# Kernel optimization log

Hardware: AMD Instinct MI355X
Metric: run time of the kernel (lower is better)

## Reference

```python
import jax, jax.numpy as jnp
import numpy as np

WH, WW = 7, 7
N = WH * WW
DIM = 384
HEADS = 12
NW = 64          # windows per image
B_ = 2048        # batch * NW


def _relative_position_index():
    ch, cw = np.meshgrid(np.arange(WH), np.arange(WW), indexing='ij')
    coords = np.stack([ch, cw]).reshape(2, -1)                      # [2, N]
    rel = coords[:, :, None] - coords[:, None, :]                   # [2, N, N]
    rel = rel.transpose(1, 2, 0)
    rel[:, :, 0] += WH - 1
    rel[:, :, 1] += WW - 1
    rel[:, :, 0] *= 2 * WW - 1
    return jnp.asarray(rel.sum(-1), dtype=jnp.int32)                # [N, N]


def setup_inputs() -> dict:
    key = jax.random.key(0)
    ks = jax.random.split(key, 7)
    return {
        'x': jax.random.normal(ks[0], (B_, N, DIM), dtype=jnp.float32),
        'qkv_w': jax.random.normal(ks[1], (3 * DIM, DIM), dtype=jnp.float32) * 0.02,
        'qkv_b': jax.random.normal(ks[2], (3 * DIM,), dtype=jnp.float32) * 0.02,
        'proj_w': jax.random.normal(ks[3], (DIM, DIM), dtype=jnp.float32) * 0.02,
        'proj_b': jax.random.normal(ks[4], (DIM,), dtype=jnp.float32) * 0.02,
        'bias_table': jax.random.normal(ks[5], ((2 * WH - 1) * (2 * WW - 1), HEADS), dtype=jnp.float32) * 0.02,
        'mask': jax.random.normal(ks[6], (NW, N, N), dtype=jnp.float32),
        'rel_idx': _relative_position_index(),
    }


def reference(x, qkv_w, qkv_b, proj_w, proj_b, bias_table, mask, rel_idx):
    B_, n, C = x.shape
    H = HEADS
    hd = C // H
    scale = hd ** (-0.5)

    qkv = x @ qkv_w.T + qkv_b                                        # [B_, N, 3C]
    qkv = qkv.reshape(B_, n, 3, H, hd).transpose(2, 0, 3, 1, 4)      # [3, B_, H, N, hd]
    q, k, v = qkv[0], qkv[1], qkv[2]

    attn = jnp.einsum('bhqd,bhkd->bhqk', q * scale, k)               # [B_, H, N, N]

    rpb = bias_table[rel_idx.reshape(-1)].reshape(n, n, H)           # gather [N, N, H]
    attn = attn + rpb.transpose(2, 0, 1)[None]                       # [B_, H, N, N]

    nW = mask.shape[0]
    attn = attn.reshape(B_ // nW, nW, H, n, n) + mask[None, :, None]
    attn = attn.reshape(B_, H, n, n)
    attn = jax.nn.softmax(attn, axis=-1)

    out = jnp.einsum('bhqk,bhkd->bhqd', attn, v)                     # [B_, H, N, hd]
    out = out.transpose(0, 2, 1, 3).reshape(B_, n, C)
    return out @ proj_w.T + proj_b
```

## Files before the change

kernel.cpp:

```cpp
#include <hip/hip_runtime.h>
#include <hip/hip_bf16.h>
#include <cstdint>
#include <cstddef>

#define NTOK 49
#define DIM 384
#define KDIM 384
#define HEADS 12
#define HD 32
#define BATCH 2048
#define MROWS (BATCH * NTOK)

typedef unsigned short u16;
typedef __bf16 bf16x8 __attribute__((ext_vector_type(8)));
typedef unsigned short u16x8 __attribute__((ext_vector_type(8)));
typedef float f32x4 __attribute__((ext_vector_type(4)));
typedef float f32x16 __attribute__((ext_vector_type(16)));

__device__ __forceinline__ u16 f2b(float f) {
  union { float f; unsigned u; } v; v.f = f;
  unsigned r = v.u + 0x7fffu + ((v.u >> 16) & 1u);
  return (u16)(r >> 16);
}

__device__ __forceinline__ bf16x8 ld_bf8(const u16* p) {
  u16x8 u = *(const u16x8*)p;
  return __builtin_bit_cast(bf16x8, u);
}

__device__ __forceinline__ void gload_lds16(const void* g, void* l) {
  __builtin_amdgcn_global_load_lds(
      (const __attribute__((address_space(1))) unsigned*)g,
      (__attribute__((address_space(3))) unsigned*)l, 16, 0, 0);
}

__global__ __launch_bounds__(256) void k_prep(const float* __restrict__ x,
                                              u16* __restrict__ xb,
                                              const float* __restrict__ qkv_w,
                                              u16* __restrict__ wqkvb,
                                              const float* __restrict__ proj_w,
                                              u16* __restrict__ wprojb,
                                              const float* __restrict__ bias_table,
                                              const float* __restrict__ mask,
                                              const int* __restrict__ rel_idx,
                                              float* __restrict__ rpbm) {
  int blk = blockIdx.x;
  if (blk < 38208) {
    const float* in;
    u16* out;
    int i;
    if (blk < 37632) {
      in = x; out = xb; i = blk * 256 + threadIdx.x;
    } else if (blk < 38064) {
      in = qkv_w; out = wqkvb; i = (blk - 37632) * 256 + threadIdx.x;
    } else {
      in = proj_w; out = wprojb; i = (blk - 38064) * 256 + threadIdx.x;
    }
    float4 v = ((const float4*)in)[i];
    ushort4 o;
    o.x = f2b(v.x); o.y = f2b(v.y); o.z = f2b(v.z); o.w = f2b(v.w);
    ((ushort4*)out)[i] = o;
  } else {
    int gidx = (blk - 38208) * 256 + threadIdx.x;
    int l    = gidx & 63;
    int rq   = (gidx >> 6) & 3;
    int tile = (gidx >> 8) & 3;
    int w    = (gidx >> 10) & 63;
    int h    = gidx >> 16;
    int mi = tile >> 1, nj = tile & 1;
    int kk0 = mi * 32 + 8 * rq + 4 * (l >> 5);
    int qq  = nj * 32 + (l & 31);
    float4 out;
    float* op = (float*)&out;
#pragma unroll
    for (int rl = 0; rl < 4; ++rl) {
      int kk = kk0 + rl;
      float v = -1e30f;
      if (kk < NTOK && qq < NTOK)
        v = bias_table[rel_idx[qq * NTOK + kk] * HEADS + h] +
            mask[(w * NTOK + qq) * NTOK + kk];
      op[rl] = v;
    }
    ((float4*)rpbm)[gidx] = out;
  }
}

template <int OUT_BF16, int NCOLS, int NTN, int GD8>
__global__ __launch_bounds__(512, 4) void k_gemm256(const u16* __restrict__ A,
                                                    const u16* __restrict__ B,
                                                    const float* __restrict__ bias,
                                                    void* __restrict__ Cv,
                                                    long m_base) {
  __shared__ u16 sh[36864];
  int bid = blockIdx.x;
  int tile = (bid & 7) * GD8 + (bid >> 3);
  int mt = tile / NTN, nt = tile - mt * NTN;
  long m0 = m_base + (long)mt * 256;
  int n0 = nt * 128;
  int tid = threadIdx.x;
  int lane = tid & 63, wid = tid >> 6;
  int wr = (wid >> 1) * 64, wc = (wid & 1) * 64;
  int c = lane & 15, g = lane >> 4;
  int gsw = (g ^ ((c >> 1) & 3)) * 8;

  int srow = wid * 16 + (lane >> 2);
  int scol = ((lane & 3) ^ ((lane >> 3) & 3)) * 8;
  const u16* gA = A + (m0 + srow) * (long)KDIM + scol;
  const u16* gB = B + (long)(n0 + srow) * KDIM + scol;
  int lrow = srow, lseg = (lane & 3) * 8;

  f32x4 acc[4][4] = {};
  bf16x8 af[4], bfr[4];

#define STAGE256(BUF, KT)                                                      \
  {                                                                            \
    u16* As_ = sh + (BUF) * 12288;                                             \
    u16* Bs_ = As_ + 8192;                                                     \
    gload_lds16(gA + (KT), &As_[lrow * 32 + lseg]);                            \
    gload_lds16(gA + (KT) + 128L * KDIM, &As_[(lrow + 128) * 32 + lseg]);      \
    gload_lds16(gB + (KT), &Bs_[lrow * 32 + lseg]);                            \
  }

#define FRAGREAD(BUF)                                                          \
  {                                                                            \
    const u16* As = sh + (BUF) * 12288;                                        \
    const u16* Bs = As + 8192;                                                 \
    _Pragma("unroll") for (int i = 0; i < 4; ++i) {                            \
      af[i]  = ld_bf8(&As[(wr + i * 16 + c) * 32 + gsw]);                      \
      bfr[i] = ld_bf8(&Bs[(wc + i * 16 + c) * 32 + gsw]);                      \
    }                                                                          \
  }

#define MFMA_CL                                                                \
  __builtin_amdgcn_s_setprio(1);                                               \
  _Pragma("unroll") for (int mi = 0; mi < 4; ++mi)                             \
  _Pragma("unroll") for (int ni = 0; ni < 4; ++ni)                             \
      acc[mi][ni] = __builtin_amdgcn_mfma_f32_16x16x32_bf16(                   \
          af[mi], bfr[ni], acc[mi][ni], 0, 0, 0);                              \
  __builtin_amdgcn_s_setprio(0);

#define GITER(T, NV)                                                           \
  {                                                                            \
    MFMA_CL;                                                                   \
    asm volatile("s_waitcnt vmcnt(" #NV ")" ::: "memory");                     \
    __builtin_amdgcn_s_barrier();                                              \
    __builtin_amdgcn_sched_barrier(0);                                         \
    if ((T) + 3 < 12) STAGE256((T) % 3, ((T) + 3) * 32);                       \
    FRAGREAD(((T) + 1) % 3);                                                   \
  }

  STAGE256(0, 0);
  STAGE256(1, 32);
  STAGE256(2, 64);
  asm volatile("s_waitcnt vmcnt(6)" ::: "memory");
  __builtin_amdgcn_s_barrier();
  __builtin_amdgcn_sched_barrier(0);
  FRAGREAD(0);

  GITER(0, 3)  GITER(1, 3)  GITER(2, 3)  GITER(3, 3)
  GITER(4, 3)  GITER(5, 3)  GITER(6, 3)  GITER(7, 3)
  GITER(8, 3)  GITER(9, 3)  GITER(10, 0)
  { MFMA_CL; }
  __builtin_amdgcn_s_barrier();
#undef GITER
#undef MFMA_CL
#undef FRAGREAD
#undef STAGE256

  if (OUT_BF16) {
    u16* C = (u16*)Cv;
#pragma unroll
    for (int mi = 0; mi < 4; ++mi)
#pragma unroll
      for (int ni = 0; ni < 4; ++ni) {
        int col = wc + ni * 16 + c;
        float bv = bias[n0 + col];
#pragma unroll
        for (int r = 0; r < 4; ++r) {
          int row = wr + mi * 16 + g * 4 + r;
          sh[row * 128 + col] = f2b(acc[mi][ni][r] + bv);
        }
      }
    __syncthreads();
#pragma unroll
    for (int rep = 0; rep < 8; ++rep) {
      int idx = rep * 4096 + tid * 8;
      int row = idx >> 7, col = idx & 127;
      int grow = (int)m0 + row;
      int b = grow / 49, tok = grow - b * 49;
      int gcol = n0 + col;
      int t = gcol / 384;
      int hc = gcol - t * 384;
      int h = hc >> 5, d0 = hc & 31;
      size_t off = (((size_t)(t * 12 + h) * BATCH + b) * 49 + tok) * 32 + d0;
      *(u16x8*)(C + off) = *(const u16x8*)&sh[idx];
    }
  } else {
    float* C = (float*)Cv;
    float* shf = (float*)sh;
#pragma unroll
    for (int chunk = 0; chunk < 2; ++chunk) {
      __syncthreads();
      if ((wid >> 2) == chunk) {
#pragma unroll
        for (int mi = 0; mi < 4; ++mi)
#pragma unroll
          for (int ni = 0; ni < 4; ++ni) {
            int col = wc + ni * 16 + c;
            float bv = bias[n0 + col];
#pragma unroll
            for (int r = 0; r < 4; ++r) {
              int lr = ((wid >> 1) & 1) * 64 + mi * 16 + g * 4 + r;
              shf[lr * 128 + col] = acc[mi][ni][r] + bv;
            }
          }
      }
      __syncthreads();
#pragma unroll
      for (int rep = 0; rep < 8; ++rep) {
        int idx = rep * 2048 + tid * 4;
        int row = idx >> 7, col = idx & 127;
        *(float4*)(C + (m0 + chunk * 128 + row) * NCOLS + n0 + col) =
            *(const float4*)&shf[idx];
      }
    }
  }
}

__global__ __launch_bounds__(256) void k_attn(const u16* __restrict__ qkv,
                                              const float* __restrict__ rpbmT,
                                              u16* __restrict__ attnout) {
  __shared__ u16 vT_lds[4][32 * 64];
  int lane = threadIdx.x & 63, wid = threadIdx.x >> 6;
  int blk = blockIdx.x;
  int w = blk / 96;
  int rr = blk - w * 96;
  int j = rr / 3;
  int hb = rr - j * 3;
  int b = j * 64 + w;
  int h = hb * 4 + wid;
  int l31 = lane & 31, hi = lane >> 5;

  const u16* qh = qkv + ((size_t)(h)*BATCH + b) * (49 * 32);
  const u16* kh = qkv + ((size_t)(12 + h) * BATCH + b) * (49 * 32);
  const u16* vh = qkv + ((size_t)(24 + h) * BATCH + b) * (49 * 32);

  u16x8 vv[4];
#pragma unroll
  for (int t = 0; t < 4; ++t) {
    int idx = t * 64 + lane;
    int jj = idx >> 2, d0 = (idx & 3) * 8;
    int jr = jj < NTOK ? jj : NTOK - 1;
    vv[t] = *(const u16x8*)(vh + jr * 32 + d0);
  }
  bf16x8 kf[2][2], qf[2][2];
#pragma unroll
  for (int mi = 0; mi < 2; ++mi) {
    int row = mi * 32 + l31; if (row > NTOK - 1) row = NTOK - 1;
#pragma unroll
    for (int k2 = 0; k2 < 2; ++k2)
      kf[mi][k2] = ld_bf8(kh + row * 32 + k2 * 16 + hi * 8);
  }
#pragma unroll
  for (int nj = 0; nj < 2; ++nj) {
    int row = nj * 32 + l31; if (row > NTOK - 1) row = NTOK - 1;
#pragma unroll
    for (int k2 = 0; k2 < 2; ++k2)
      qf[nj][k2] = ld_bf8(qh + row * 32 + k2 * 16 + hi * 8);
  }

  u16* vt = vT_lds[wid];
#pragma unroll
  for (int t = 0; t < 4; ++t) {
    int idx = t * 64 + lane;
    int jj = idx >> 2, d0 = (idx & 3) * 8;
#pragma unroll
    for (int dd = 0; dd < 8; ++dd) {
      int d = d0 + dd;
      int byte = (d * 128 + jj * 2) ^ ((d & 7) << 4);
      *(u16*)((char*)vt + byte) = (u16)vv[t][dd];
    }
  }

  f32x16 s[2][2];
  f32x16 z16 = {};
#pragma unroll
  for (int mi = 0; mi < 2; ++mi)
#pragma unroll
    for (int nj = 0; nj < 2; ++nj) {
      s[mi][nj] = __builtin_amdgcn_mfma_f32_32x32x16_bf16(kf[mi][0], qf[nj][0],
                                                          z16, 0, 0, 0);
      s[mi][nj] = __builtin_amdgcn_mfma_f32_32x32x16_bf16(kf[mi][1], qf[nj][1],
                                                          s[mi][nj], 0, 0, 0);
    }

  const float scale = 0.17677669529663687f;
  const f32x4* rp = (const f32x4*)(rpbmT + ((size_t)(h * 64 + w)) * 4096);
#pragma unroll
  for (int mi = 0; mi < 2; ++mi)
#pragma unroll
    for (int nj = 0; nj < 2; ++nj)
#pragma unroll
      for (int rq = 0; rq < 4; ++rq) {
        f32x4 rv = rp[(mi * 2 + nj) * 256 + rq * 64 + lane];
#pragma unroll
        for (int rl = 0; rl < 4; ++rl)
          s[mi][nj][rq * 4 + rl] = s[mi][nj][rq * 4 + rl] * scale + rv[rl];
      }

  float inv_[2];
#pragma unroll
  for (int nj = 0; nj < 2; ++nj) {
    float mx = s[0][nj][0];
#pragma unroll
    for (int mi = 0; mi < 2; ++mi)
#pragma unroll
      for (int r = 0; r < 16; ++r)
        mx = fmaxf(mx, s[mi][nj][r]);
    mx = fmaxf(mx, __shfl_xor(mx, 32));
    float sum = 0.f;
#pragma unroll
    for (int mi = 0; mi < 2; ++mi)
#pragma unroll
      for (int r = 0; r < 16; ++r) {
        float p = __expf(s[mi][nj][r] - mx);
        s[mi][nj][r] = p;
        sum += p;
      }
    sum += __shfl_xor(sum, 32);
    inv_[nj] = __builtin_amdgcn_rcpf(sum);
  }

  asm volatile("s_waitcnt lgkmcnt(0)" ::: "memory");
  __builtin_amdgcn_sched_barrier(0);

  f32x16 o[2] = {};
#pragma unroll
  for (int kk = 0; kk < 4; ++kk) {
    int byte = (l31 * 128 + kk * 32 + hi * 16) ^ ((l31 & 7) << 4);
    bf16x8 va = __builtin_bit_cast(bf16x8, *(const u16x8*)((const char*)vt + byte));
#pragma unroll
    for (int nj = 0; nj < 2; ++nj) {
      const int mi = kk >> 1, br = (kk & 1) * 8;
      unsigned t0, t1, t2, t3;
      asm("v_cvt_pk_bf16_f32 %0, %1, %2"
          : "=v"(t0) : "v"(s[mi][nj][br + 0]), "v"(s[mi][nj][br + 1]));
      asm("v_cvt_pk_bf16_f32 %0, %1, %2"
          : "=v"(t1) : "v"(s[mi][nj][br + 2]), "v"(s[mi][nj][br + 3]));
      asm("v_cvt_pk_bf16_f32 %0, %1, %2"
          : "=v"(t2) : "v"(s[mi][nj][br + 4]), "v"(s[mi][nj][br + 5]));
      asm("v_cvt_pk_bf16_f32 %0, %1, %2"
          : "=v"(t3) : "v"(s[mi][nj][br + 6]), "v"(s[mi][nj][br + 7]));
      asm("v_permlane32_swap_b32 %0, %1" : "+v"(t0), "+v"(t2));
      asm("v_permlane32_swap_b32 %0, %1" : "+v"(t1), "+v"(t3));
      uint4 uu; uu.x = t0; uu.y = t1; uu.z = t2; uu.w = t3;
      bf16x8 pb = __builtin_bit_cast(bf16x8, uu);
      o[nj] = __builtin_amdgcn_mfma_f32_32x32x16_bf16(va, pb, o[nj], 0, 0, 0);
    }
  }

  u16* obase = attnout + (size_t)b * (NTOK * DIM) + h * HD;
#pragma unroll
  for (int nj = 0; nj < 2; ++nj) {
    int q = nj * 32 + l31;
    if (q < NTOK) {
#pragma unroll
      for (int r = 0; r < 16; ++r) {
        int d = (r & 3) + 8 * (r >> 2) + 4 * hi;
        obase[(size_t)q * DIM + d] = f2b(o[nj][r] * inv_[nj]);
      }
    }
  }
}

extern "C" void kernel_launch(void* const* d_in, const int* in_sizes, int n_in,
                              void* d_out, int out_size, void* d_ws, size_t ws_size,
                              hipStream_t stream) {
  const float* x       = (const float*)d_in[0];
  const float* qkv_w   = (const float*)d_in[1];
  const float* qkv_b   = (const float*)d_in[2];
  const float* proj_w  = (const float*)d_in[3];
  const float* proj_b  = (const float*)d_in[4];
  const float* bias_tb = (const float*)d_in[5];
  const float* mask    = (const float*)d_in[6];
  const int*   rel_idx = (const int*)d_in[7];
  float* out = (float*)d_out;

  char* ws = (char*)d_ws;
  u16*   xb      = (u16*)(ws + 0);
  u16*   wqkvb   = (u16*)(ws + 77070336);
  u16*   wprojb  = (u16*)(ws + 77955072);
  float* rpbm    = (float*)(ws + 78249984);
  u16*   qkv     = (u16*)(ws + 90832896);
  u16*   attnout = (u16*)(ws + 322043904);

  k_prep<<<41280, 256, 0, stream>>>(x, xb, qkv_w, wqkvb, proj_w, wprojb,
                                    bias_tb, mask, rel_idx, rpbm);

  k_gemm256<1, 1152, 9, 225><<<1800, 512, 0, stream>>>(xb, wqkvb, qkv_b,
                                                       (void*)qkv, 0L);
  k_gemm256<1, 1152, 9, 216><<<1728, 512, 0, stream>>>(xb, wqkvb, qkv_b,
                                                       (void*)qkv, 51200L);

  k_attn<<<6144, 256, 0, stream>>>(qkv, rpbm, attnout);

  k_gemm256<0, 384, 3, 147><<<1176, 512, 0, stream>>>(attnout, wprojb, proj_b,
                                                      (void*)out, 0L);

  (void)in_sizes; (void)n_in; (void)out_size; (void)ws_size;
}
```

Measured before the change: 354.1 us.

## Write V pre-transposed from QKV GEMM and drop LDS transpose in attention

The QKV GEMM epilogue now writes the V third transposed, as [head][batch][d][token padded to 56], through a swizzled LDS staging step. The attention kernel then loads V fragments straight from global memory, with no per-wave LDS transpose or waitcnt barrier. The 49th token is handled by a separate mostly-zero MFMA, and output stores become 4-wide vectors. The two QKV GEMM launches are merged into one, and attnout reuses the xb workspace region. The trade-off is scalar 2-byte global stores in the V epilogue, which may be uncoalesced and slow.

```diff
diff --git a/kernel.cpp b/kernel.cpp
--- a/kernel.cpp
+++ b/kernel.cpp
@@ -10,6 +10,7 @@
 #define HD 32
 #define BATCH 2048
 #define MROWS (BATCH * NTOK)
+#define VPAD 56
 
 typedef unsigned short u16;
 typedef __bf16 bf16x8 __attribute__((ext_vector_type(8)));
@@ -90,12 +91,12 @@
                                                     const u16* __restrict__ B,
                                                     const float* __restrict__ bias,
                                                     void* __restrict__ Cv,
-                                                    long m_base) {
+                                                    u16* __restrict__ Cv2) {
   __shared__ u16 sh[36864];
   int bid = blockIdx.x;
   int tile = (bid & 7) * GD8 + (bid >> 3);
   int mt = tile / NTN, nt = tile - mt * NTN;
-  long m0 = m_base + (long)mt * 256;
+  long m0 = (long)mt * 256;
   int n0 = nt * 128;
   int tid = threadIdx.x;
   int lane = tid & 63, wid = tid >> 6;
@@ -168,32 +169,66 @@
 #undef STAGE256
 
   if (OUT_BF16) {
-    u16* C = (u16*)Cv;
-#pragma unroll
-    for (int mi = 0; mi < 4; ++mi)
-#pragma unroll
-      for (int ni = 0; ni < 4; ++ni) {
-        int col = wc + ni * 16 + c;
-        float bv = bias[n0 + col];
-#pragma unroll
-        for (int r = 0; r < 4; ++r) {
-          int row = wr + mi * 16 + g * 4 + r;
-          sh[row * 128 + col] = f2b(acc[mi][ni][r] + bv);
+    if (n0 < 768) {
+      u16* C = (u16*)Cv;
+#pragma unroll
+      for (int mi = 0; mi < 4; ++mi)
+#pragma unroll
+        for (int ni = 0; ni < 4; ++ni) {
+          int col = wc + ni * 16 + c;
+          float bv = bias[n0 + col];
+#pragma unroll
+          for (int r = 0; r < 4; ++r) {
+            int row = wr + mi * 16 + g * 4 + r;
+            sh[row * 128 + col] = f2b(acc[mi][ni][r] + bv);
+          }
         }
-      }
-    __syncthreads();
-#pragma unroll
-    for (int rep = 0; rep < 8; ++rep) {
-      int idx = rep * 4096 + tid * 8;
-      int row = idx >> 7, col = idx & 127;
-      int grow = (int)m0 + row;
-      int b = grow / 49, tok = grow - b * 49;
-      int gcol = n0 + col;
-      int t = gcol / 384;
-      int hc = gcol - t * 384;
-      int h = hc >> 5, d0 = hc & 31;
-      size_t off = (((size_t)(t * 12 + h) * BATCH + b) * 49 + tok) * 32 + d0;
-      *(u16x8*)(C + off) = *(const u16x8*)&sh[idx];
+      __syncthreads();
+#pragma unroll
+      for (int rep = 0; rep < 8; ++rep) {
+        int idx = rep * 4096 + tid * 8;
+        int row = idx >> 7, col = idx & 127;
+        int grow = (int)m0 + row;
+        int b = grow / 49, tok = grow - b * 49;
+        int gcol = n0 + col;
+        int t = gcol / 384;
+        int hc = gcol - t * 384;
+        int h = hc >> 5, d0 = hc & 31;
+        size_t off = (((size_t)(t * 12 + h) * BATCH + b) * 49 + tok) * 32 + d0;
+        *(u16x8*)(C + off) = *(const u16x8*)&sh[idx];
+      }
+    } else {
+#pragma unroll
+      for (int mi = 0; mi < 4; ++mi)
+#pragma unroll
+        for (int ni = 0; ni < 4; ++ni) {
+          int col = wc + ni * 16 + c;
+          float bv = bias[n0 + col];
+          int sw = (col & 7) << 3;
+#pragma unroll
+          for (int r = 0; r < 4; ++r) {
+            int row = wr + mi * 16 + g * 4 + r;
+            sh[col * 256 + (row ^ sw)] = f2b(acc[mi][ni][r] + bv);
+          }
+        }
+      __syncthreads();
+#pragma unroll
+      for (int rep = 0; rep < 8; ++rep) {
+        int idx = rep * 4096 + tid * 8;
+        int dloc = idx >> 8, rowb = idx & 255;
+        u16x8 vals = *(const u16x8*)&sh[dloc * 256 + (rowb ^ ((dloc & 7) << 3))];
+        int hcol = n0 - 768 + dloc;
+        int h = hcol >> 5, d = hcol & 31;
+        int grow = (int)m0 + rowb;
+        int b = grow / 49, j = grow - b * 49;
+        size_t off = ((size_t)(h * BATCH + b) * 32 + d) * VPAD + j;
+#pragma unroll
+        for (int e = 0; e < 8; ++e) {
+          Cv2[off] = (u16)vals[e];
+          ++j; ++off;
+          if (j == 49) { j = 0; ++b; off += (size_t)32 * VPAD - 49; }
+        }
+      }
     }
   } else {
     float* C = (float*)Cv;
@@ -227,10 +262,10 @@
   }
 }
 
-__global__ __launch_bounds__(256) void k_attn(const u16* __restrict__ qkv,
+__global__ __launch_bounds__(256) void k_attn(const u16* __restrict__ qkvqk,
+                                              const u16* __restrict__ vtg,
                                               const float* __restrict__ rpbmT,
                                               u16* __restrict__ attnout) {
-  __shared__ u16 vT_lds[4][32 * 64];
   int lane = threadIdx.x & 63, wid = threadIdx.x >> 6;
   int blk = blockIdx.x;
   int w = blk / 96;
@@ -241,18 +276,16 @@
   int h = hb * 4 + wid;
   int l31 = lane & 31, hi = lane >> 5;
 
-  const u16* qh = qkv + ((size_t)(h)*BATCH + b) * (49 * 32);
-  const u16* kh = qkv + ((size_t)(12 + h) * BATCH + b) * (49 * 32);
-  const u16* vh = qkv + ((size_t)(24 + h) * BATCH + b) * (49 * 32);
-
-  u16x8 vv[4];
-#pragma unroll
-  for (int t = 0; t < 4; ++t) {
-    int idx = t * 64 + lane;
-    int jj = idx >> 2, d0 = (idx & 3) * 8;
-    int jr = jj < NTOK ? jj : NTOK - 1;
-    vv[t] = *(const u16x8*)(vh + jr * 32 + d0);
-  }
+  const u16* qh = qkvqk + ((size_t)(h)*BATCH + b) * (49 * 32);
+  const u16* kh = qkvqk + ((size_t)(12 + h) * BATCH + b) * (49 * 32);
+  const u16* vt = vtg + ((size_t)(h)*BATCH + b) * (32 * VPAD);
+
+  bf16x8 va[3];
+#pragma unroll
+  for (int kk = 0; kk < 3; ++kk)
+    va[kk] = ld_bf8(vt + l31 * VPAD + kk * 16 + hi * 8);
+  u16 v48 = vt[l31 * VPAD + 48];
+
   bf16x8 kf[2][2], qf[2][2];
 #pragma unroll
   for (int mi = 0; mi < 2; ++mi) {
@@ -267,19 +300,6 @@
 #pragma unroll
     for (int k2 = 0; k2 < 2; ++k2)
       qf[nj][k2] = ld_bf8(qh + row * 32 + k2 * 16 + hi * 8);
-  }
-
-  u16* vt = vT_lds[wid];
-#pragma unroll
-  for (int t = 0; t < 4; ++t) {
-    int idx = t * 64 + lane;
-    int jj = idx >> 2, d0 = (idx & 3) * 8;
-#pragma unroll
-    for (int dd = 0; dd < 8; ++dd) {
-      int d = d0 + dd;
-      int byte = (d * 128 + jj * 2) ^ ((d & 7) << 4);
-      *(u16*)((char*)vt + byte) = (u16)vv[t][dd];
-    }
   }
 
   f32x16 s[2][2];
@@ -331,14 +351,9 @@
     inv_[nj] = __builtin_amdgcn_rcpf(sum);
   }
 
-  asm volatile("s_waitcnt lgkmcnt(0)" ::: "memory");
-  __builtin_amdgcn_sched_barrier(0);
-
   f32x16 o[2] = {};
 #pragma unroll
-  for (int kk = 0; kk < 4; ++kk) {
-    int byte = (l31 * 128 + kk * 32 + hi * 16) ^ ((l31 & 7) << 4);
-    bf16x8 va = __builtin_bit_cast(bf16x8, *(const u16x8*)((const char*)vt + byte));
+  for (int kk = 0; kk < 3; ++kk) {
 #pragma unroll
     for (int nj = 0; nj < 2; ++nj) {
       const int mi = kk >> 1, br = (kk & 1) * 8;
@@ -355,7 +370,20 @@
       asm("v_permlane32_swap_b32 %0, %1" : "+v"(t1), "+v"(t3));
       uint4 uu; uu.x = t0; uu.y = t1; uu.z = t2; uu.w = t3;
       bf16x8 pb = __builtin_bit_cast(bf16x8, uu);
-      o[nj] = __builtin_amdgcn_mfma_f32_32x32x16_bf16(va, pb, o[nj], 0, 0, 0);
+      o[nj] = __builtin_amdgcn_mfma_f32_32x32x16_bf16(va[kk], pb, o[nj], 0, 0, 0);
+    }
+  }
+  {
+    uint4 a3u = {0u, 0u, 0u, 0u};
+    a3u.x = (hi == 0) ? (unsigned)v48 : 0u;
+    bf16x8 va3 = __builtin_bit_cast(bf16x8, a3u);
+#pragma unroll
+    for (int nj = 0; nj < 2; ++nj) {
+      u16 p48 = f2b(s[1][nj][8]);
+      uint4 p3u = {0u, 0u, 0u, 0u};
+      p3u.x = (hi == 0) ? (unsigned)p48 : 0u;
+      bf16x8 pb3 = __builtin_bit_cast(bf16x8, p3u);
+      o[nj] = __builtin_amdgcn_mfma_f32_32x32x16_bf16(va3, pb3, o[nj], 0, 0, 0);
     }
   }
 
@@ -365,9 +393,13 @@
     int q = nj * 32 + l31;
     if (q < NTOK) {
 #pragma unroll
-      for (int r = 0; r < 16; ++r) {
-        int d = (r & 3) + 8 * (r >> 2) + 4 * hi;
-        obase[(size_t)q * DIM + d] = f2b(o[nj][r] * inv_[nj]);
+      for (int q4 = 0; q4 < 4; ++q4) {
+        ushort4 ov;
+        ov.x = f2b(o[nj][q4 * 4 + 0] * inv_[nj]);
+        ov.y = f2b(o[nj][q4 * 4 + 1] * inv_[nj]);
+        ov.z = f2b(o[nj][q4 * 4 + 2] * inv_[nj]);
+        ov.w = f2b(o[nj][q4 * 4 + 3] * inv_[nj]);
+        *(ushort4*)(obase + (size_t)q * DIM + q4 * 8 + hi * 4) = ov;
       }
     }
   }
@@ -388,24 +420,23 @@
 
   char* ws = (char*)d_ws;
   u16*   xb      = (u16*)(ws + 0);
+  u16*   attnout = (u16*)(ws + 0);
   u16*   wqkvb   = (u16*)(ws + 77070336);
   u16*   wprojb  = (u16*)(ws + 77955072);
   float* rpbm    = (float*)(ws + 78249984);
-  u16*   qkv     = (u16*)(ws + 90832896);
-  u16*   attnout = (u16*)(ws + 322043904);
+  u16*   qkvqk   = (u16*)(ws + 90832896);
+  u16*   vtg     = (u16*)(ws + 244973568);
 
   k_prep<<<41280, 256, 0, stream>>>(x, xb, qkv_w, wqkvb, proj_w, wprojb,
                                     bias_tb, mask, rel_idx, rpbm);
 
-  k_gemm256<1, 1152, 9, 225><<<1800, 512, 0, stream>>>(xb, wqkvb, qkv_b,
-                                                       (void*)qkv, 0L);
-  k_gemm256<1, 1152, 9, 216><<<1728, 512, 0, stream>>>(xb, wqkvb, qkv_b,
-                                                       (void*)qkv, 51200L);
-
-  k_attn<<<6144, 256, 0, stream>>>(qkv, rpbm, attnout);
+  k_gemm256<1, 1152, 9, 441><<<3528, 512, 0, stream>>>(xb, wqkvb, qkv_b,
+                                                       (void*)qkvqk, vtg);
+
+  k_attn<<<6144, 256, 0, stream>>>(qkvqk, vtg, rpbm, attnout);
 
   k_gemm256<0, 384, 3, 147><<<1176, 512, 0, stream>>>(attnout, wprojb, proj_b,
-                                                      (void*)out, 0L);
+                                                      (void*)out, nullptr);
 
   (void)in_sizes; (void)n_in; (void)out_size; (void)ws_size;
 }
```

New measurement: 380.1 us. +7.3%, slower.

## Load V directly into MFMA operand layout, drop LDS transpose, merge QKV GEMM launches

Applied to the files above, without the earlier changes.

The attention kernel no longer stages V through a swizzled LDS transpose. Each lane gathers V elements straight from global memory with strided 16-bit loads, and the PV MFMA operands are swapped so the output comes out in a different register layout. Softmax normalization is applied to the probabilities before the bf16 conversion rather than to the output, and the output stores are reindexed. The two QKV GEMM launches are merged into a single 3528-block launch, which removes the m_base parameter. This saves LDS traffic and a launch, but the scalar strided V loads and narrower output stores may cost memory efficiency.

```diff
diff --git a/kernel.cpp b/kernel.cpp
--- a/kernel.cpp
+++ b/kernel.cpp
@@ -89,13 +89,12 @@
 __global__ __launch_bounds__(512, 4) void k_gemm256(const u16* __restrict__ A,
                                                     const u16* __restrict__ B,
                                                     const float* __restrict__ bias,
-                                                    void* __restrict__ Cv,
-                                                    long m_base) {
+                                                    void* __restrict__ Cv) {
   __shared__ u16 sh[36864];
   int bid = blockIdx.x;
   int tile = (bid & 7) * GD8 + (bid >> 3);
   int mt = tile / NTN, nt = tile - mt * NTN;
-  long m0 = m_base + (long)mt * 256;
+  long m0 = (long)mt * 256;
   int n0 = nt * 128;
   int tid = threadIdx.x;
   int lane = tid & 63, wid = tid >> 6;
@@ -230,7 +229,6 @@
 __global__ __launch_bounds__(256) void k_attn(const u16* __restrict__ qkv,
                                               const float* __restrict__ rpbmT,
                                               u16* __restrict__ attnout) {
-  __shared__ u16 vT_lds[4][32 * 64];
   int lane = threadIdx.x & 63, wid = threadIdx.x >> 6;
   int blk = blockIdx.x;
   int w = blk / 96;
@@ -245,14 +243,16 @@
   const u16* kh = qkv + ((size_t)(12 + h) * BATCH + b) * (49 * 32);
   const u16* vh = qkv + ((size_t)(24 + h) * BATCH + b) * (49 * 32);
 
-  u16x8 vv[4];
-#pragma unroll
-  for (int t = 0; t < 4; ++t) {
-    int idx = t * 64 + lane;
-    int jj = idx >> 2, d0 = (idx & 3) * 8;
-    int jr = jj < NTOK ? jj : NTOK - 1;
-    vv[t] = *(const u16x8*)(vh + jr * 32 + d0);
-  }
+  bf16x8 vb[4];
+#pragma unroll
+  for (int kk = 0; kk < 4; ++kk) {
+    u16x8 tmp;
+#pragma unroll
+    for (int e = 0; e < 8; ++e)
+      tmp[e] = vh[(kk * 16 + hi * 8 + e) * 32 + l31];
+    vb[kk] = __builtin_bit_cast(bf16x8, tmp);
+  }
+
   bf16x8 kf[2][2], qf[2][2];
 #pragma unroll
   for (int mi = 0; mi < 2; ++mi) {
@@ -267,19 +267,6 @@
 #pragma unroll
     for (int k2 = 0; k2 < 2; ++k2)
       qf[nj][k2] = ld_bf8(qh + row * 32 + k2 * 16 + hi * 8);
-  }
-
-  u16* vt = vT_lds[wid];
-#pragma unroll
-  for (int t = 0; t < 4; ++t) {
-    int idx = t * 64 + lane;
-    int jj = idx >> 2, d0 = (idx & 3) * 8;
-#pragma unroll
-    for (int dd = 0; dd < 8; ++dd) {
-      int d = d0 + dd;
-      int byte = (d * 128 + jj * 2) ^ ((d & 7) << 4);
-      *(u16*)((char*)vt + byte) = (u16)vv[t][dd];
-    }
   }
 
   f32x16 s[2][2];
@@ -308,7 +295,6 @@
           s[mi][nj][rq * 4 + rl] = s[mi][nj][rq * 4 + rl] * scale + rv[rl];
       }
 
-  float inv_[2];
 #pragma unroll
   for (int nj = 0; nj < 2; ++nj) {
     float mx = s[0][nj][0];
@@ -328,17 +314,17 @@
         sum += p;
       }
     sum += __shfl_xor(sum, 32);
-    inv_[nj] = __builtin_amdgcn_rcpf(sum);
-  }
-
-  asm volatile("s_waitcnt lgkmcnt(0)" ::: "memory");
-  __builtin_amdgcn_sched_barrier(0);
+    float inv = __builtin_amdgcn_rcpf(sum);
+#pragma unroll
+    for (int mi = 0; mi < 2; ++mi)
+#pragma unroll
+      for (int r = 0; r < 16; ++r)
+        s[mi][nj][r] *= inv;
+  }
 
   f32x16 o[2] = {};
 #pragma unroll
   for (int kk = 0; kk < 4; ++kk) {
-    int byte = (l31 * 128 + kk * 32 + hi * 16) ^ ((l31 & 7) << 4);
-    bf16x8 va = __builtin_bit_cast(bf16x8, *(const u16x8*)((const char*)vt + byte));
 #pragma unroll
     for (int nj = 0; nj < 2; ++nj) {
       const int mi = kk >> 1, br = (kk & 1) * 8;
@@ -354,23 +340,20 @@
       asm("v_permlane32_swap_b32 %0, %1" : "+v"(t0), "+v"(t2));
       asm("v_permlane32_swap_b32 %0, %1" : "+v"(t1), "+v"(t3));
       uint4 uu; uu.x = t0; uu.y = t1; uu.z = t2; uu.w = t3;
-      bf16x8 pb = __builtin_bit_cast(bf16x8, uu);
-      o[nj] = __builtin_amdgcn_mfma_f32_32x32x16_bf16(va, pb, o[nj], 0, 0, 0);
+      bf16x8 pa = __builtin_bit_cast(bf16x8, uu);
+      o[nj] = __builtin_amdgcn_mfma_f32_32x32x16_bf16(pa, vb[kk], o[nj], 0, 0, 0);
     }
   }
 
   u16* obase = attnout + (size_t)b * (NTOK * DIM) + h * HD;
 #pragma unroll
-  for (int nj = 0; nj < 2; ++nj) {
-    int q = nj * 32 + l31;
-    if (q < NTOK) {
-#pragma unroll
-      for (int r = 0; r < 16; ++r) {
-        int d = (r & 3) + 8 * (r >> 2) + 4 * hi;
-        obase[(size_t)q * DIM + d] = f2b(o[nj][r] * inv_[nj]);
-      }
-    }
-  }
+  for (int nj = 0; nj < 2; ++nj)
+#pragma unroll
+    for (int r = 0; r < 16; ++r) {
+      int q = nj * 32 + (r & 3) + 8 * (r >> 2) + 4 * hi;
+      if (q < NTOK)
+        obase[(size_t)q * DIM + l31] = f2b(o[nj][r]);
+    }
 }
 
 extern "C" void kernel_launch(void* const* d_in, const int* in_sizes, int n_in,
@@ -397,15 +380,13 @@
   k_prep<<<41280, 256, 0, stream>>>(x, xb, qkv_w, wqkvb, proj_w, wprojb,
                                     bias_tb, mask, rel_idx, rpbm);
 
-  k_gemm256<1, 1152, 9, 225><<<1800, 512, 0, stream>>>(xb, wqkvb, qkv_b,
-                                                       (void*)qkv, 0L);
-  k_gemm256<1, 1152, 9, 216><<<1728, 512, 0, stream>>>(xb, wqkvb, qkv_b,
-                                                       (void*)qkv, 51200L);
+  k_gemm256<1, 1152, 9, 441><<<3528, 512, 0, stream>>>(xb, wqkvb, qkv_b,
+                                                       (void*)qkv);
 
   k_attn<<<6144, 256, 0, stream>>>(qkv, rpbm, attnout);
 
   k_gemm256<0, 384, 3, 147><<<1176, 512, 0, stream>>>(attnout, wprojb, proj_b,
-                                                      (void*)out, 0L);
+                                                      (void*)out);
 
   (void)in_sizes; (void)n_in; (void)out_size; (void)ws_size;
 }
```

Result: faster. 343.8 us (-2.9%).
